# Optimization experiments

Hardware: AMD Instinct MI355X
Metric: run time of the kernel (lower is better)

## Reference

```python
import jax, jax.numpy as jnp
import numpy as np

N_NODES = 50000
N_EDGES = 800000
F_IN = 128
HID = 128
F_ADD = 32
N_GRAPHS = 128


def setup_inputs() -> dict:
    key = jax.random.key(0)
    ks = jax.random.split(key, 12)
    x = jax.random.normal(ks[0], (N_NODES, F_IN), dtype=jnp.float32)
    edge_index = jax.random.randint(ks[1], (2, N_EDGES), 0, N_NODES, dtype=jnp.int64)
    batch = jnp.sort(jax.random.randint(ks[2], (N_NODES,), 0, N_GRAPHS, dtype=jnp.int64))
    additional_features = jax.random.normal(ks[3], (N_GRAPHS, F_ADD), dtype=jnp.float32)
    def glorot(k, shape):
        fan_in, fan_out = shape[0], shape[1]
        lim = jnp.sqrt(6.0 / (fan_in + fan_out)).astype(jnp.float32)
        return jax.random.uniform(k, shape, jnp.float32, -lim, lim)
    W1 = glorot(ks[4], (F_IN, HID)); b1 = jnp.zeros((HID,), jnp.float32)
    W2 = glorot(ks[5], (HID, HID)); b2 = jnp.zeros((HID,), jnp.float32)
    fc1_w = glorot(ks[6], (HID + F_ADD, HID)); fc1_b = jnp.zeros((HID,), jnp.float32)
    fc2_w = glorot(ks[7], (HID, 2)); fc2_b = jnp.zeros((2,), jnp.float32)
    return {"x": x, "edge_index": edge_index, "batch": batch,
            "additional_features": additional_features,
            "W1": W1, "b1": b1, "W2": W2, "b2": b2,
            "fc1_w": fc1_w, "fc1_b": fc1_b, "fc2_w": fc2_w, "fc2_b": fc2_b}


def _gcn_conv(h, src, dst, norm, W, b):
    # h: [N, d_in]; symmetric-normalized scatter-add aggregation (PyG GCNConv)
    h = h @ W                                   # [N, d_out]
    msg = h[src] * norm[:, None]                # gather + scale: [E+N, d_out]
    return jax.ops.segment_sum(msg, dst, num_segments=N_NODES) + b


def reference(x, edge_index, batch, additional_features,
              W1, b1, W2, b2, fc1_w, fc1_b, fc2_w, fc2_b):
    loops = jnp.arange(N_NODES, dtype=edge_index.dtype)
    src = jnp.concatenate([edge_index[0], loops])   # A + I
    dst = jnp.concatenate([edge_index[1], loops])
    deg = jax.ops.segment_sum(jnp.ones_like(src, dtype=x.dtype), dst,
                              num_segments=N_NODES)
    dinv = jnp.where(deg > 0, jax.lax.rsqrt(jnp.maximum(deg, 1.0)), 0.0)
    norm = dinv[src] * dinv[dst]

    h = jax.nn.relu(_gcn_conv(x, src, dst, norm, W1, b1))
    h = jax.nn.relu(_gcn_conv(h, src, dst, norm, W2, b2))
    # dropout is identity in eval mode

    sums = jax.ops.segment_sum(h, batch, num_segments=N_GRAPHS)    # [G, HID]
    counts = jax.ops.segment_sum(jnp.ones((N_NODES,), h.dtype), batch,
                                 num_segments=N_GRAPHS)
    pooled = sums / jnp.maximum(counts, 1.0)[:, None]              # global_mean_pool

    z = jnp.concatenate([pooled, additional_features], axis=1)     # [G, HID+F_ADD]
    z = jax.nn.relu(z @ fc1_w + fc1_b)
    return z @ fc2_w + fc2_b                                       # [G, 2]
```

## Files before the change

kernel.cpp:

```cpp
#include <hip/hip_runtime.h>

#define NN 50000
#define NE 800000
#define FD 128
#define FDH 64
#define FA 32
#define NG 128
#define EETOT (NE + NN)
#define NBLK ((NN + 255) / 256)
#define PK 8
#define FEPB 2048
#define FNCH ((EETOT + FEPB - 1) / FEPB)
#define NPXCD 6250

typedef __attribute__((ext_vector_type(8))) short short8;
typedef __attribute__((ext_vector_type(4))) float f32x4;

__device__ __forceinline__ float bfbits(unsigned short u) {
    return __uint_as_float(((unsigned int)u) << 16);
}
__device__ __forceinline__ float bflo(unsigned int p) { return __uint_as_float(p << 16); }
__device__ __forceinline__ float bfhi(unsigned int p) { return __uint_as_float(p & 0xffff0000u); }
__device__ __forceinline__ unsigned short f2bf(float f) {
    unsigned int u = __float_as_uint(f);
    unsigned int r = u + 0x7FFFu + ((u >> 16) & 1u);
    return (unsigned short)(r >> 16);
}
__device__ __forceinline__ unsigned int packbf(float a, float b) {
    return (unsigned int)f2bf(a) | ((unsigned int)f2bf(b) << 16);
}
__device__ __forceinline__ int ld_idx(const int* p, int i, int is64) {
    return is64 ? p[2 * i] : p[i];
}
__device__ int probe_bf16(const unsigned int* t, int nwords) {
    int nz = 0, hits = 0;
    for (int i = 0; i < nwords; ++i) {
        unsigned int w = t[i];
        if (w == 0u) continue;
        ++nz;
        unsigned int e = (w >> 7) & 0xFFu;
        if (e >= 100u && e <= 140u) ++hits;
    }
    return (nz < 8) ? 1 : (hits * 4 >= nz * 3);
}

__global__ __launch_bounds__(128) void mark_kernel(float* out, float v) {
    out[threadIdx.x] = v;
}

__global__ __launch_bounds__(64) void flags_kernel(
        const unsigned int* x, const int* ei, const int* batch,
        const unsigned int* addf, const unsigned int* w1, const unsigned int* b1,
        const unsigned int* w2, const unsigned int* b2, const unsigned int* fc1w,
        const unsigned int* fc1b, const unsigned int* fc2w, const unsigned int* fc2b,
        int* flags) {
    if (threadIdx.x != 0) return;
    flags[0]  = probe_bf16(x, 64);
    flags[3]  = probe_bf16(addf, 64);
    flags[4]  = probe_bf16(w1, 64);
    flags[5]  = probe_bf16(b1, 64);
    flags[6]  = probe_bf16(w2, 64);
    flags[7]  = probe_bf16(b2, 64);
    flags[8]  = probe_bf16(fc1w, 64);
    flags[9]  = probe_bf16(fc1b, 64);
    flags[10] = probe_bf16(fc2w, 64);
    flags[11] = probe_bf16(fc2b, 1);
    int odd_or = 0;
    for (int k = 0; k < 32; ++k) odd_or |= ei[2 * k + 1];
    flags[12] = (odd_or == 0) ? 1 : 0;
    flags[13] = (batch[NN - 1] == 0) ? 1 : 0;
}

__global__ __launch_bounds__(256) void prep(
        const void* x, const void* addf,
        const void* w1, const void* b1, const void* w2, const void* b2,
        const void* fc1w, const void* fc1b, const void* fc2w, const void* fc2b,
        unsigned int* bufC, unsigned int* W1t, unsigned int* W2t,
        float* addff, float* b1f, float* b2f, float* fc1wf, float* fc1bf,
        float* fc2wf, float* fc2bf, const int* flags, int* degi) {
    int b = blockIdx.x;
    if (b < 12500) {
        int i = b * 256 + threadIdx.x;
        if (flags[0]) {
            bufC[i] = ((const unsigned int*)x)[i];
        } else {
            const float* s = (const float*)x;
            bufC[i] = packbf(s[2 * i], s[2 * i + 1]);
        }
    } else if (b < 12564) {
        int rel = (b - 12500) * 256 + threadIdx.x;
        const void* src = (rel < 8192) ? w1 : w2;
        unsigned int* dst = (rel < 8192) ? W1t : W2t;
        int flag = (rel < 8192) ? flags[4] : flags[6];
        int rr = rel & 8191;
        int n = rr >> 6, kk = rr & 63;
        float lo, hi;
        if (flag) {
            const unsigned short* s = (const unsigned short*)src;
            lo = bfbits(s[(2 * kk) * FD + n]);
            hi = bfbits(s[(2 * kk + 1) * FD + n]);
        } else {
            const float* s = (const float*)src;
            lo = s[(2 * kk) * FD + n];
            hi = s[(2 * kk + 1) * FD + n];
        }
        dst[rr] = packbf(lo, hi);
    } else if (b < 12663) {
        int i = (b - 12564) * 256 + threadIdx.x;
        const void* src; float* dst; int flag; int rel;
        if      (i < 4096)  { src = addf; dst = addff; flag = flags[3];  rel = i; }
        else if (i < 4224)  { src = b1;   dst = b1f;   flag = flags[5];  rel = i - 4096; }
        else if (i < 4352)  { src = b2;   dst = b2f;   flag = flags[7];  rel = i - 4224; }
        else if (i < 24832) { src = fc1w; dst = fc1wf; flag = flags[8];  rel = i - 4352; }
        else if (i < 24960) { src = fc1b; dst = fc1bf; flag = flags[9];  rel = i - 24832; }
        else if (i < 25216) { src = fc2w; dst = fc2wf; flag = flags[10]; rel = i - 24960; }
        else if (i < 25218) { src = fc2b; dst = fc2bf; flag = flags[11]; rel = i - 25216; }
        else return;
        if (flag) dst[rel] = bfbits(((const unsigned short*)src)[rel]);
        else      dst[rel] = ((const float*)src)[rel];
    } else {
        int i = (b - 12663) * 256 + threadIdx.x;
        if (i < NN) degi[i] = 0;
    }
}

__global__ __launch_bounds__(256) void deg_kernel(const int* ei, const int* flags,
                                                  int* deg) {
    int e = blockIdx.x * 256 + threadIdx.x;
    int is64 = flags[12];
    if (e < NE) atomicAdd(&deg[ld_idx(ei, NE + e, is64)], 1);
}

__global__ __launch_bounds__(256) void scan1(const int* deg, float* dinv,
                                             int* escan, int* bsum) {
    __shared__ int sh[256];
    int i = blockIdx.x * 256 + threadIdx.x;
    int d = (i < NN) ? deg[i] : 0;
    if (i < NN) dinv[i] = rsqrtf((float)(d + 1));
    int v = (i < NN) ? d + 1 : 0;
    sh[threadIdx.x] = v;
    __syncthreads();
    for (int off = 1; off < 256; off <<= 1) {
        int a = ((int)threadIdx.x >= off) ? sh[threadIdx.x - off] : 0;
        __syncthreads();
        sh[threadIdx.x] += a;
        __syncthreads();
    }
    if (i < NN) escan[i] = sh[threadIdx.x] - v;
    if (threadIdx.x == 255) bsum[blockIdx.x] = sh[255];
}

__global__ __launch_bounds__(256) void scan3(const int* escan, const int* bsum,
        const int* batch, const int* flags, int* rowstart, int* cursor, int* gstart) {
    __shared__ int sb[256];
    int t = threadIdx.x;
    int v = (t < NBLK) ? bsum[t] : 0;
    sb[t] = v;
    __syncthreads();
    for (int off = 1; off < 256; off <<= 1) {
        int a = (t >= off) ? sb[t - off] : 0;
        __syncthreads();
        sb[t] += a;
        __syncthreads();
    }
    int boff = (blockIdx.x == 0) ? 0 : sb[blockIdx.x - 1];
    int i = blockIdx.x * 256 + t;
    if (i < NN) {
        int r = escan[i] + boff;
        rowstart[i] = r;
        cursor[i]   = r;
    }
    if (i == 0) rowstart[NN] = EETOT;
    if (i < NN) {
        int is64 = flags[13];
        int bc = ld_idx(batch, i, is64);
        if (i == 0) {
            for (int g = 0; g <= bc; ++g) gstart[g] = 0;
        } else {
            int bp = ld_idx(batch, i - 1, is64);
            for (int g = bp + 1; g <= bc; ++g) gstart[g] = i;
        }
        if (i == NN - 1) {
            for (int g = bc + 1; g <= NG; ++g) gstart[g] = NN;
        }
    }
}

__global__ __launch_bounds__(256) void fill_kernel(const int* ei, const int* flags,
        const float* dinv, int* cursor, unsigned int* cv) {
    int chunk = blockIdx.x >> 3;
    int par   = blockIdx.x & 7;
    int base  = chunk * FEPB;
    int is64  = flags[12];
    #pragma unroll
    for (int k = 0; k < FEPB / 256; ++k) {
        int e = base + k * 256 + threadIdx.x;
        if (e >= EETOT) break;
        int s, d;
        if (e < NE) { d = ld_idx(ei, NE + e, is64); s = -1; }
        else        { s = d = e - NE; }
        if (d / NPXCD != par) continue;
        if (s < 0) s = ld_idx(ei, e, is64);
        int pos = atomicAdd(&cursor[d], 1);
        cv[pos] = (unsigned int)s | ((unsigned int)f2bf(dinv[s] * dinv[d]) << 16);
    }
}

__global__ __launch_bounds__(256) void gemm_mfma(const unsigned int* __restrict__ A,
        const unsigned int* __restrict__ Wt, unsigned short* __restrict__ C) {
    int wave = threadIdx.x >> 6;
    int lane = threadIdx.x & 63;
    int quad = lane >> 4;
    int l16  = lane & 15;
    int mbase = blockIdx.x * 64 + wave * 16;
    int ra = mbase + l16;
    if (ra >= NN) ra = NN - 1;
    short8 af[4];
    const uint4* Arow = (const uint4*)(A + (size_t)ra * FDH);
    #pragma unroll
    for (int kk = 0; kk < 4; ++kk) {
        uint4 v = Arow[kk * 4 + quad];
        af[kk] = *(short8*)&v;
    }
    #pragma unroll
    for (int nt = 0; nt < 8; ++nt) {
        int n = nt * 16 + l16;
        const uint4* Wrow = (const uint4*)(Wt + (size_t)n * FDH);
        f32x4 acc = {0.f, 0.f, 0.f, 0.f};
        #pragma unroll
        for (int kk = 0; kk < 4; ++kk) {
            uint4 wv = Wrow[kk * 4 + quad];
            short8 bf = *(short8*)&wv;
            acc = __builtin_amdgcn_mfma_f32_16x16x32_bf16(af[kk], bf, acc, 0, 0, 0);
        }
        int row0 = mbase + quad * 4;
        #pragma unroll
        for (int reg = 0; reg < 4; ++reg) {
            int r = row0 + reg;
            if (r < NN) C[(size_t)r * FD + nt * 16 + l16] = f2bf(acc[reg]);
        }
    }
}

__global__ __launch_bounds__(256) void aggregate_kernel(const unsigned int* Hb,
        const unsigned int* cv, const int* rowstart, const float* bias,
        unsigned int* outb) {
    int n = blockIdx.x * 4 + (threadIdx.x >> 6);
    int cp = threadIdx.x & 63;
    if (n >= NN) return;
    int jb = rowstart[n], je = rowstart[n + 1];
    float acc0 = 0.f, acc1 = 0.f;
    int j = jb;
    for (; j + 7 < je; j += 8) {
        unsigned int rr[8], hh[8];
        #pragma unroll
        for (int k = 0; k < 8; ++k) rr[k] = cv[j + k];
        #pragma unroll
        for (int k = 0; k < 8; ++k) hh[k] = Hb[(size_t)(rr[k] & 0xFFFFu) * FDH + cp];
        #pragma unroll
        for (int k = 0; k < 8; ++k) {
            float v = bfbits((unsigned short)(rr[k] >> 16));
            acc0 += v * bflo(hh[k]);
            acc1 += v * bfhi(hh[k]);
        }
    }
    for (; j + 3 < je; j += 4) {
        unsigned int rr[4], hh[4];
        #pragma unroll
        for (int k = 0; k < 4; ++k) rr[k] = cv[j + k];
        #pragma unroll
        for (int k = 0; k < 4; ++k) hh[k] = Hb[(size_t)(rr[k] & 0xFFFFu) * FDH + cp];
        #pragma unroll
        for (int k = 0; k < 4; ++k) {
            float v = bfbits((unsigned short)(rr[k] >> 16));
            acc0 += v * bflo(hh[k]);
            acc1 += v * bfhi(hh[k]);
        }
    }
    for (; j < je; ++j) {
        unsigned int r = cv[j];
        unsigned int h = Hb[(size_t)(r & 0xFFFFu) * FDH + cp];
        float v = bfbits((unsigned short)(r >> 16));
        acc0 += v * bflo(h);
        acc1 += v * bfhi(h);
    }
    acc0 = fmaxf(acc0 + bias[2 * cp], 0.f);
    acc1 = fmaxf(acc1 + bias[2 * cp + 1], 0.f);
    outb[(size_t)n * FDH + cp] = packbf(acc0, acc1);
}

__global__ __launch_bounds__(64) void pool_part(const unsigned int* Hb,
        const int* gstart, float* part) {
    int g = blockIdx.x >> 3;
    int k = blockIdx.x & (PK - 1);
    int cp = threadIdx.x;
    int s = gstart[g], e = gstart[g + 1];
    int len = e - s;
    int per = (len + PK - 1) / PK;
    int ss = s + k * per;
    int ee = ss + per; if (ee > e) ee = e;
    float a0 = 0.f, a1 = 0.f, b0 = 0.f, b1 = 0.f;
    int n = ss;
    for (; n + 1 < ee; n += 2) {
        unsigned int h0 = Hb[(size_t)n * FDH + cp];
        unsigned int h1 = Hb[(size_t)(n + 1) * FDH + cp];
        a0 += bflo(h0); a1 += bfhi(h0);
        b0 += bflo(h1); b1 += bfhi(h1);
    }
    if (n < ee) {
        unsigned int h0 = Hb[(size_t)n * FDH + cp];
        a0 += bflo(h0); a1 += bfhi(h0);
    }
    part[(size_t)(g * PK + k) * FD + 2 * cp]     = a0 + b0;
    part[(size_t)(g * PK + k) * FD + 2 * cp + 1] = a1 + b1;
}

__global__ __launch_bounds__(128) void head_kernel(const float* part, const int* gstart,
        const float* addf, const float* fc1w, const float* fc1b,
        const float* fc2w, const float* fc2b, const int* flags, void* outp) {
    int g = blockIdx.x;
    int t = threadIdx.x;
    __shared__ float z[FD + FA];
    __shared__ float h[FD];
    float a = 0.f;
    #pragma unroll
    for (int k = 0; k < PK; ++k) a += part[(size_t)(g * PK + k) * FD + t];
    float cnt = (float)(gstart[g + 1] - gstart[g]);
    if (cnt < 1.0f) cnt = 1.0f;
    z[t] = a / cnt;
    if (t < FA) z[FD + t] = addf[g * FA + t];
    __syncthreads();
    float acc = fc1b[t];
    #pragma unroll 4
    for (int k = 0; k < FD + FA; ++k)
        acc += z[k] * fc1w[k * FD + t];
    h[t] = fmaxf(acc, 0.f);
    __syncthreads();
    if (t < 2) {
        float o = fc2b[t];
        for (int j = 0; j < FD; ++j) o += h[j] * fc2w[j * 2 + t];
        if (flags[0]) ((unsigned short*)outp)[g * 2 + t] = f2bf(o);
        else          ((float*)outp)[g * 2 + t] = o;
    }
}

extern "C" void kernel_launch(void* const* d_in, const int* in_sizes, int n_in,
                              void* d_out, int out_size, void* d_ws, size_t ws_size,
                              hipStream_t stream) {
    (void)out_size;

    if (n_in != 12) {
        hipLaunchKernelGGL(mark_kernel, dim3(1), dim3(128), 0, stream,
                           (float*)d_out, 2000.0f);
        return;
    }
    const int exp_sizes[12] = {6400000, 1600000, 50000, 4096, 16384, 128,
                               16384, 128, 20480, 128, 256, 2};
    for (int i = 0; i < 12; ++i) {
        if (in_sizes[i] != exp_sizes[i]) {
            hipLaunchKernelGGL(mark_kernel, dim3(1), dim3(128), 0, stream,
                               (float*)d_out, 3000.0f + 100.0f * i);
            return;
        }
    }

    size_t off = 0;
    char* base = (char*)d_ws;
#define WSALLOC(ptr, type, nbytes) \
    type* ptr = (type*)(base + off); off += (((size_t)(nbytes)) + 255) & ~(size_t)255;
    WSALLOC(bufA,  unsigned int, (size_t)NN * FDH * 4)
    WSALLOC(bufB,  unsigned int, (size_t)NN * FDH * 4)
    WSALLOC(bufC,  unsigned int, (size_t)NN * FDH * 4)
    WSALLOC(dinv,  float, (size_t)NN * 4)
    WSALLOC(degi,  int,   (size_t)NN * 4)
    WSALLOC(rowst, int,   (size_t)(NN + 1) * 4)
    WSALLOC(cursor,int,   (size_t)NN * 4)
    WSALLOC(escan, int,   (size_t)NN * 4)
    WSALLOC(bsum,  int,   (size_t)NBLK * 4)
    WSALLOC(cv,    unsigned int, (size_t)EETOT * 4)
    WSALLOC(part,  float, (size_t)NG * PK * FD * 4)
    WSALLOC(gstart,int,   (size_t)(NG + 1) * 4)
    WSALLOC(W1t,   unsigned int, (size_t)FD * FDH * 4)
    WSALLOC(W2t,   unsigned int, (size_t)FD * FDH * 4)
    WSALLOC(b1f,   float, FD * 4)
    WSALLOC(b2f,   float, FD * 4)
    WSALLOC(addff, float, (size_t)NG * FA * 4)
    WSALLOC(fc1wf, float, (size_t)(FD + FA) * FD * 4)
    WSALLOC(fc1bf, float, FD * 4)
    WSALLOC(fc2wf, float, FD * 2 * 4)
    WSALLOC(fc2bf, float, 2 * 4)
    WSALLOC(flags, int, 16 * 4)
#undef WSALLOC
    if (ws_size < off) {
        hipLaunchKernelGGL(mark_kernel, dim3(1), dim3(128), 0, stream,
                           (float*)d_out, 1000.0f);
        return;
    }

    const int* ei    = (const int*)d_in[1];
    const int* batch = (const int*)d_in[2];

    hipLaunchKernelGGL(flags_kernel, dim3(1), dim3(64), 0, stream,
                       (const unsigned int*)d_in[0], ei, batch,
                       (const unsigned int*)d_in[3], (const unsigned int*)d_in[4],
                       (const unsigned int*)d_in[5], (const unsigned int*)d_in[6],
                       (const unsigned int*)d_in[7], (const unsigned int*)d_in[8],
                       (const unsigned int*)d_in[9], (const unsigned int*)d_in[10],
                       (const unsigned int*)d_in[11], flags);

    hipLaunchKernelGGL(prep, dim3(12859), dim3(256), 0, stream,
                       d_in[0], d_in[3], d_in[4], d_in[5], d_in[6],
                       d_in[7], d_in[8], d_in[9], d_in[10], d_in[11],
                       bufC, W1t, W2t, addff, b1f, b2f, fc1wf, fc1bf,
                       fc2wf, fc2bf, flags, degi);

    hipLaunchKernelGGL(deg_kernel, dim3((NE + 255) / 256), dim3(256), 0, stream,
                       ei, flags, degi);
    hipLaunchKernelGGL(scan1, dim3(NBLK), dim3(256), 0, stream,
                       degi, dinv, escan, bsum);
    hipLaunchKernelGGL(scan3, dim3(NBLK), dim3(256), 0, stream,
                       escan, bsum, batch, flags, rowst, cursor, gstart);
    hipLaunchKernelGGL(fill_kernel, dim3(FNCH * 8), dim3(256), 0, stream,
                       ei, flags, dinv, cursor, cv);

    hipLaunchKernelGGL(gemm_mfma, dim3((NN + 63) / 64), dim3(256), 0, stream,
                       bufC, W1t, (unsigned short*)bufA);
    hipLaunchKernelGGL(aggregate_kernel, dim3((NN + 3) / 4), dim3(256), 0, stream,
                       bufA, cv, rowst, b1f, bufB);
    hipLaunchKernelGGL(gemm_mfma, dim3((NN + 63) / 64), dim3(256), 0, stream,
                       bufB, W2t, (unsigned short*)bufA);
    hipLaunchKernelGGL(aggregate_kernel, dim3((NN + 3) / 4), dim3(256), 0, stream,
                       bufA, cv, rowst, b2f, bufB);

    hipLaunchKernelGGL(pool_part, dim3(NG * PK), dim3(64), 0, stream,
                       bufB, gstart, part);
    hipLaunchKernelGGL(head_kernel, dim3(NG), dim3(FD), 0, stream,
                       part, gstart, addff, fc1wf, fc1bf, fc2wf, fc2bf,
                       flags, d_out);
}
```

Measured before the change: 338.7 us.

## Split aggregation edges across two wavefronts per node and XCD-partition degree atomics

The aggregate kernel now gives each node two 64-lane wavefronts, each summing half of the node's edge list, and combines the halves through LDS before bias and ReLU. The aim is more memory-level parallelism for the latency-bound gather. The degree kernel switches to chunked blocks with eight partitions, each handling only destinations in one slice of nodes, so atomics stay local to one XCD's L2. In exchange every edge index is read eight times in deg_kernel, and aggregation adds a block-wide barrier and halves the number of nodes per block.

```diff
diff --git a/kernel.cpp b/kernel.cpp
--- a/kernel.cpp
+++ b/kernel.cpp
@@ -11,6 +11,7 @@
 #define PK 8
 #define FEPB 2048
 #define FNCH ((EETOT + FEPB - 1) / FEPB)
+#define DNCH ((NE + FEPB - 1) / FEPB)
 #define NPXCD 6250
 
 typedef __attribute__((ext_vector_type(8))) short short8;
@@ -126,9 +127,18 @@
 
 __global__ __launch_bounds__(256) void deg_kernel(const int* ei, const int* flags,
                                                   int* deg) {
-    int e = blockIdx.x * 256 + threadIdx.x;
-    int is64 = flags[12];
-    if (e < NE) atomicAdd(&deg[ld_idx(ei, NE + e, is64)], 1);
+    int chunk = blockIdx.x >> 3;
+    int par   = blockIdx.x & 7;
+    int base  = chunk * FEPB;
+    int is64  = flags[12];
+    #pragma unroll
+    for (int k = 0; k < FEPB / 256; ++k) {
+        int e = base + k * 256 + threadIdx.x;
+        if (e >= NE) break;
+        int d = ld_idx(ei, NE + e, is64);
+        if (d / NPXCD != par) continue;
+        atomicAdd(&deg[d], 1);
+    }
 }
 
 __global__ __launch_bounds__(256) void scan1(const int* deg, float* dinv,
@@ -245,13 +255,18 @@
 __global__ __launch_bounds__(256) void aggregate_kernel(const unsigned int* Hb,
         const unsigned int* cv, const int* rowstart, const float* bias,
         unsigned int* outb) {
-    int n = blockIdx.x * 4 + (threadIdx.x >> 6);
-    int cp = threadIdx.x & 63;
-    if (n >= NN) return;
+    __shared__ float lds[2 * FD];
+    int tid  = threadIdx.x;
+    int node = tid >> 7;
+    int half = (tid >> 6) & 1;
+    int cp   = tid & 63;
+    int n = blockIdx.x * 2 + node;
     int jb = rowstart[n], je = rowstart[n + 1];
+    int mid = jb + ((je - jb + 1) >> 1);
+    int j  = half ? mid : jb;
+    int j1 = half ? je  : mid;
     float acc0 = 0.f, acc1 = 0.f;
-    int j = jb;
-    for (; j + 7 < je; j += 8) {
+    for (; j + 7 < j1; j += 8) {
         unsigned int rr[8], hh[8];
         #pragma unroll
         for (int k = 0; k < 8; ++k) rr[k] = cv[j + k];
@@ -264,7 +279,7 @@
             acc1 += v * bfhi(hh[k]);
         }
     }
-    for (; j + 3 < je; j += 4) {
+    for (; j + 3 < j1; j += 4) {
         unsigned int rr[4], hh[4];
         #pragma unroll
         for (int k = 0; k < 4; ++k) rr[k] = cv[j + k];
@@ -277,16 +292,25 @@
             acc1 += v * bfhi(hh[k]);
         }
     }
-    for (; j < je; ++j) {
+    for (; j < j1; ++j) {
         unsigned int r = cv[j];
         unsigned int h = Hb[(size_t)(r & 0xFFFFu) * FDH + cp];
         float v = bfbits((unsigned short)(r >> 16));
         acc0 += v * bflo(h);
         acc1 += v * bfhi(h);
     }
-    acc0 = fmaxf(acc0 + bias[2 * cp], 0.f);
-    acc1 = fmaxf(acc1 + bias[2 * cp + 1], 0.f);
-    outb[(size_t)n * FDH + cp] = packbf(acc0, acc1);
+    if (half) {
+        lds[node * FD + 2 * cp]     = acc0;
+        lds[node * FD + 2 * cp + 1] = acc1;
+    }
+    __syncthreads();
+    if (!half) {
+        acc0 += lds[node * FD + 2 * cp];
+        acc1 += lds[node * FD + 2 * cp + 1];
+        acc0 = fmaxf(acc0 + bias[2 * cp], 0.f);
+        acc1 = fmaxf(acc1 + bias[2 * cp + 1], 0.f);
+        outb[(size_t)n * FDH + cp] = packbf(acc0, acc1);
+    }
 }
 
 __global__ __launch_bounds__(64) void pool_part(const unsigned int* Hb,
@@ -414,7 +438,7 @@
                        bufC, W1t, W2t, addff, b1f, b2f, fc1wf, fc1bf,
                        fc2wf, fc2bf, flags, degi);
 
-    hipLaunchKernelGGL(deg_kernel, dim3((NE + 255) / 256), dim3(256), 0, stream,
+    hipLaunchKernelGGL(deg_kernel, dim3(DNCH * 8), dim3(256), 0, stream,
                        ei, flags, degi);
     hipLaunchKernelGGL(scan1, dim3(NBLK), dim3(256), 0, stream,
                        degi, dinv, escan, bsum);
@@ -425,11 +449,11 @@
 
     hipLaunchKernelGGL(gemm_mfma, dim3((NN + 63) / 64), dim3(256), 0, stream,
                        bufC, W1t, (unsigned short*)bufA);
-    hipLaunchKernelGGL(aggregate_kernel, dim3((NN + 3) / 4), dim3(256), 0, stream,
+    hipLaunchKernelGGL(aggregate_kernel, dim3(NN / 2), dim3(256), 0, stream,
                        bufA, cv, rowst, b1f, bufB);
     hipLaunchKernelGGL(gemm_mfma, dim3((NN + 63) / 64), dim3(256), 0, stream,
                        bufB, W2t, (unsigned short*)bufA);
-    hipLaunchKernelGGL(aggregate_kernel, dim3((NN + 3) / 4), dim3(256), 0, stream,
+    hipLaunchKernelGGL(aggregate_kernel, dim3(NN / 2), dim3(256), 0, stream,
                        bufA, cv, rowst, b2f, bufB);
 
     hipLaunchKernelGGL(pool_part, dim3(NG * PK), dim3(64), 0, stream,
```

New measurement: 365.0 us. 1.08x slower.
